# Kernel optimization log

Measured on AMD Instinct MI355X. Metric: run time of the kernel, lower is better.

Reference implementation:

```python
import jax, jax.numpy as jnp
import numpy as np

NL, DM, DI, DS, DR, DC = 4, 1024, 2048, 16, 64, 4
B, L, DLOC, NC = 8, 224, 672, 10
EPS = 1e-5


def _rmsnorm(h, w):
    return h * jax.lax.rsqrt(jnp.mean(h * h, axis=-1, keepdims=True) + EPS) * w


def setup_inputs() -> dict:
    key = jax.random.key(0)
    ks = jax.random.split(key, 10)
    s = 0.02
    return dict(
        x=jax.random.normal(ks[0], (B, L, DLOC), jnp.float32),
        w_proj=jax.random.normal(ks[1], (DLOC, DM), jnp.float32) * s,
        b_proj=jnp.zeros((DM,), jnp.float32),
        norm_w=jnp.ones((NL, DM), jnp.float32),
        w_in=jax.random.normal(ks[2], (NL, DM, 2 * DI), jnp.float32) * s,
        w_conv=jax.random.normal(ks[3], (NL, DI, DC), jnp.float32) * s,
        b_conv=jnp.zeros((NL, DI), jnp.float32),
        w_x=jax.random.normal(ks[4], (NL, DI, DR + 2 * DS), jnp.float32) * s,
        w_dt=jax.random.normal(ks[5], (NL, DR, DI), jnp.float32) * s,
        b_dt=jax.random.normal(ks[6], (NL, DI), jnp.float32) * 0.1,
        A_log=jnp.broadcast_to(jnp.log(jnp.arange(1, DS + 1, dtype=jnp.float32)), (NL, DI, DS)) + jnp.zeros((NL, DI, DS), jnp.float32),
        Dp=jnp.ones((NL, DI), jnp.float32),
        w_out=jax.random.normal(ks[7], (NL, DI, DM), jnp.float32) * s,
        final_norm_w=jnp.ones((DM,), jnp.float32),
        w_fc=jax.random.normal(ks[8], (DM, NC), jnp.float32) * s,
        b_fc=jnp.zeros((NC,), jnp.float32),
    )


def reference(x, w_proj, b_proj, norm_w, w_in, w_conv, b_conv, w_x, w_dt, b_dt, A_log, Dp, w_out, final_norm_w, w_fc, b_fc):
    # input_proj: (B,L,DLOC) -> (B,L,DM)
    h = x @ w_proj + b_proj
    for l in range(NL):
        xn = _rmsnorm(h, norm_w[l])
        xz = xn @ w_in[l]                      # (B,L,2*DI)
        xp, z = jnp.split(xz, 2, axis=-1)
        # causal depthwise conv1d along L, kernel size DC
        xpad = jnp.pad(xp, ((0, 0), (DC - 1, 0), (0, 0)))
        xc = sum(xpad[:, k:k + L, :] * w_conv[l][:, k] for k in range(DC)) + b_conv[l]
        xc = jax.nn.silu(xc)
        x_dbl = xc @ w_x[l]                    # (B,L,DR+2*DS)
        dtr, Bm, Cm = jnp.split(x_dbl, [DR, DR + DS], axis=-1)
        dt = jax.nn.softplus(dtr @ w_dt[l] + b_dt[l])   # (B,L,DI)
        A = -jnp.exp(A_log[l])                 # (DI,DS)
        xs = (jnp.swapaxes(dt, 0, 1), jnp.swapaxes(Bm, 0, 1),
              jnp.swapaxes(Cm, 0, 1), jnp.swapaxes(xc, 0, 1))

        def step(hs, inp):
            dt_t, B_t, C_t, u_t = inp          # (B,DI),(B,DS),(B,DS),(B,DI)
            dA = jnp.exp(dt_t[:, :, None] * A)                        # (B,DI,DS)
            hs = dA * hs + (dt_t * u_t)[:, :, None] * B_t[:, None, :]
            y = jnp.einsum('bds,bs->bd', hs, C_t)
            return hs, y

        h0 = jnp.zeros((B, DI, DS), x.dtype)
        _, ys = jax.lax.scan(step, h0, xs)     # ys: (L,B,DI)
        y = jnp.swapaxes(ys, 0, 1) + Dp[l] * xc
        y = y * jax.nn.silu(z)
        h = h + y @ w_out[l]
    h = _rmsnorm(h, final_norm_w)
    pooled = h[:, -1, :]                       # last-token pooling
    return pooled @ w_fc + b_fc                # (B,NC)
```

## Files before the change

### kernel.cpp

```cpp
#include <hip/hip_runtime.h>
#include <hip/hip_bf16.h>
#include <hip/hip_fp16.h>
#include <math.h>

#define NL 4
#define DM 1024
#define DI 2048
#define DS 16
#define DR 64
#define DC 4
#define B_ 8
#define L_ 224
#define DLOC 672
#define NC 10
#define EPS 1e-5f

#define ROWS (B_ * L_)
#define NCHK 14
#define CHS 16

typedef unsigned short u16;
typedef __attribute__((ext_vector_type(8))) short bf16x8;
typedef __attribute__((ext_vector_type(4))) float f32x4;
typedef __attribute__((address_space(1))) const void gvoid_t;
typedef __attribute__((address_space(3))) void lvoid_t;

__device__ __forceinline__ u16 f2bf(float f) {
  union { float f; unsigned int u; } v;
  v.f = f;
  unsigned int u = v.u;
  return (u16)((u + 0x7fffu + ((u >> 16) & 1u)) >> 16);
}

__device__ __forceinline__ void load4h(const __half* p, float* o) {
  uint2 r = *(const uint2*)p;
  __half2 h0 = *(__half2*)&r.x;
  __half2 h1 = *(__half2*)&r.y;
  float2 f0 = __half22float2(h0);
  float2 f1 = __half22float2(h1);
  o[0] = f0.x; o[1] = f0.y; o[2] = f1.x; o[3] = f1.y;
}

template <int ACC, int BROW, int TSTORE, int ACT, int SPLITK, typename OT>
__global__ __launch_bounds__(256) void gemm_bt_mfma(
    const u16* __restrict__ A, const u16* __restrict__ Bt,
    const float* __restrict__ bias, OT* __restrict__ C, int K, int lda,
    int ldb, int ldc) {
  if (SPLITK) {
    A += (size_t)blockIdx.z * SPLITK;
    Bt += (size_t)blockIdx.z * SPLITK;
  }
  __shared__ __align__(16) u16 As[2][128 * 32];
  __shared__ __align__(16) u16 Bs[2][128 * 32];
  const int tid = threadIdx.x;
  const int lane = tid & 63;
  const int wv = tid >> 6;
  const int n0 = blockIdx.x * 128;
  const int m0 = blockIdx.y * 128;
  const int wm0 = (wv & 1) * 64;
  const int wn0 = (wv >> 1) * 64;
  const int quad = lane >> 4;
  const int l16 = lane & 15;

  const int srow = wv * 32 + (lane >> 2);
  const int scol = (lane & 3) * 8;
  const u16* ga0 = A + (size_t)(m0 + srow) * lda + scol;
  const u16* ga1 = ga0 + (size_t)16 * lda;
  const u16* gb0 = Bt + (size_t)(n0 + srow) * ldb + scol;
  const u16* gb1 = gb0 + (size_t)16 * ldb;
  const int lo0 = (wv * 32) * 32;
  const int lo1 = (wv * 32 + 16) * 32;

  f32x4 acc[4][4] = {};

  auto STAGE = [&](int buf, int kk) {
    __builtin_amdgcn_global_load_lds((gvoid_t*)(ga0 + kk),
                                     (lvoid_t*)&As[buf][lo0], 16, 0, 0);
    __builtin_amdgcn_global_load_lds((gvoid_t*)(ga1 + kk),
                                     (lvoid_t*)&As[buf][lo1], 16, 0, 0);
    __builtin_amdgcn_global_load_lds((gvoid_t*)(gb0 + kk),
                                     (lvoid_t*)&Bs[buf][lo0], 16, 0, 0);
    __builtin_amdgcn_global_load_lds((gvoid_t*)(gb1 + kk),
                                     (lvoid_t*)&Bs[buf][lo1], 16, 0, 0);
  };

  const int NT = K >> 5;
  STAGE(0, 0);
  __syncthreads();
  for (int t = 0; t < NT; ++t) {
    const int cur = t & 1;
    if (t + 1 < NT) STAGE(cur ^ 1, (t + 1) << 5);
    bf16x8 af[4], bfr[4];
#pragma unroll
    for (int i = 0; i < 4; i++)
      af[i] = *(const bf16x8*)&As[cur][(wm0 + i * 16 + l16) * 32 + quad * 8];
#pragma unroll
    for (int j = 0; j < 4; j++)
      bfr[j] = *(const bf16x8*)&Bs[cur][(wn0 + j * 16 + l16) * 32 + quad * 8];
#pragma unroll
    for (int i = 0; i < 4; i++)
#pragma unroll
      for (int j = 0; j < 4; j++)
        acc[i][j] = __builtin_amdgcn_mfma_f32_16x16x32_bf16(af[i], bfr[j],
                                                            acc[i][j], 0, 0, 0);
    __syncthreads();
  }

#pragma unroll
  for (int i = 0; i < 4; i++) {
#pragma unroll
    for (int j = 0; j < 4; j++) {
      const int col = n0 + wn0 + j * 16 + l16;
      const int rowb = m0 + wm0 + i * 16 + quad * 4;
      if (TSTORE) {
        __half* Ch = (__half*)C;
        union { __half2 h[2]; uint2 u; } pk;
        pk.h[0].x = __float2half(acc[i][j][0]);
        pk.h[0].y = __float2half(acc[i][j][1]);
        pk.h[1].x = __float2half(acc[i][j][2]);
        pk.h[1].y = __float2half(acc[i][j][3]);
        *(uint2*)(Ch + (size_t)col * ldc + rowb) = pk.u;
      } else {
        float bv = 0.f;
        if (BROW == 1) bv = bias[col];
#pragma unroll
        for (int r = 0; r < 4; r++) {
          float v = acc[i][j][r] + bv;
          if (BROW == 2) v += bias[rowb + r];
          if (ACT == 1) v = (v > 20.f) ? v : log1pf(expf(v));
          OT* p = C + (size_t)(rowb + r) * ldc + col;
          if (ACC == 2) {
            atomicAdd((float*)p, v);
          } else {
            if (ACC == 1) v += (float)*p;
            *p = (OT)v;
          }
        }
      }
    }
  }
}

__device__ __forceinline__ void transpose_cvt_body(
    const float* __restrict__ src, u16* __restrict__ dst, int K, int N,
    int bx, int by, int tid) {
  __shared__ float t[32][33];
  const int n0 = bx * 32;
  const int k0 = by * 32;
  const int c = tid & 31;
  const int r = tid >> 5;
#pragma unroll
  for (int rr = 0; rr < 4; rr++)
    t[r + rr * 8][c] = src[(size_t)(k0 + r + rr * 8) * N + n0 + c];
  __syncthreads();
#pragma unroll
  for (int rr = 0; rr < 4; rr++)
    dst[(size_t)(n0 + r + rr * 8) * K + k0 + c] = f2bf(t[c][r + rr * 8]);
}

__global__ __launch_bounds__(256) void transpose_cvt_kernel(
    const float* __restrict__ src, u16* __restrict__ dst, int K, int N) {
  transpose_cvt_body(src, dst, K, N, blockIdx.x, blockIdx.y, threadIdx.x);
}

__global__ __launch_bounds__(256) void prep_weights_kernel(
    const float* __restrict__ w_in_l, const float* __restrict__ w_out_l,
    const float* __restrict__ w_x_l, const float* __restrict__ w_dt_l,
    u16* __restrict__ winT, u16* __restrict__ woutT, u16* __restrict__ w_x16,
    u16* __restrict__ w_dt16) {
  int bid = blockIdx.x;
  if (bid < 4096) {
    transpose_cvt_body(w_in_l, winT, DM, 2 * DI, bid & 127, bid >> 7,
                       threadIdx.x);
  } else if (bid < 6144) {
    bid -= 4096;
    transpose_cvt_body(w_out_l, woutT, DI, DM, bid & 31, bid >> 5,
                       threadIdx.x);
  } else if (bid < 6336) {
    bid -= 6144;
    transpose_cvt_body(w_x_l, w_x16, DI, 96, bid % 3, bid / 3, threadIdx.x);
  } else {
    bid -= 6336;
    transpose_cvt_body(w_dt_l, w_dt16, DR, DI, bid & 63, bid >> 6,
                       threadIdx.x);
  }
}

__global__ __launch_bounds__(256) void cvt_kernel(const float* __restrict__ src,
                                                  u16* __restrict__ dst) {
  const int i = blockIdx.x * 256 + threadIdx.x;
  const float4 v = ((const float4*)src)[i];
  ushort4 o;
  o.x = f2bf(v.x);
  o.y = f2bf(v.y);
  o.z = f2bf(v.z);
  o.w = f2bf(v.w);
  ((ushort4*)dst)[i] = o;
}

__global__ __launch_bounds__(256) void init_bias_kernel(
    const float* __restrict__ b, float* __restrict__ h) {
  const int i = blockIdx.x * 256 + threadIdx.x;
  const float4 v = ((const float4*)b)[i & (DM / 4 - 1)];
  ((float4*)h)[i] = v;
}

__global__ __launch_bounds__(256) void rmsnorm_kernel(
    const float* __restrict__ h, const float* __restrict__ w,
    u16* __restrict__ out) {
  const int row = blockIdx.x;
  const int tid = threadIdx.x;
  const float4 v = *(const float4*)(h + (size_t)row * DM + tid * 4);
  float ss = v.x * v.x + v.y * v.y + v.z * v.z + v.w * v.w;
#pragma unroll
  for (int off = 32; off > 0; off >>= 1) ss += __shfl_xor(ss, off);
  __shared__ float red[4];
  if ((tid & 63) == 0) red[tid >> 6] = ss;
  __syncthreads();
  float tot = red[0] + red[1] + red[2] + red[3];
  const float inv = rsqrtf(tot / (float)DM + EPS);
  const float4 wv = *(const float4*)(w + tid * 4);
  ushort4 o;
  o.x = f2bf(v.x * inv * wv.x);
  o.y = f2bf(v.y * inv * wv.y);
  o.z = f2bf(v.z * inv * wv.z);
  o.w = f2bf(v.w * inv * wv.w);
  *(ushort4*)(out + (size_t)row * DM + tid * 4) = o;
}

__global__ __launch_bounds__(256) void conv_silu_tile_kernel(
    const __half* __restrict__ xpT, const float* __restrict__ wc,
    const float* __restrict__ bc, __half* __restrict__ uT,
    u16* __restrict__ u16rm) {
  __shared__ u16 tile[32][33];
  const int tid = threadIdx.x;
  const int d0 = blockIdx.x * 32;
  const int r0 = blockIdx.y * 32;
  const int dl = tid >> 3;
  const int rq = (tid & 7) * 4;
  const int d = d0 + dl;
  const int r = r0 + rq;
  const int t = r % L_;
  const __half* row = xpT + (size_t)d * ROWS + r;
  float v[4];
  load4h(row, v);
  float p0 = 0.f, p1 = 0.f, p2 = 0.f;
  if (t > 0) {
    p0 = __half2float(row[-3]);
    p1 = __half2float(row[-2]);
    p2 = __half2float(row[-1]);
  }
  const float w0 = wc[d * 4 + 0], w1 = wc[d * 4 + 1], w2 = wc[d * 4 + 2],
              w3 = wc[d * 4 + 3];
  const float bb = bc[d];
  float o[4];
  float s;
  s = bb + p0 * w0 + p1 * w1 + p2 * w2 + v[0] * w3; o[0] = s / (1.f + expf(-s));
  s = bb + p1 * w0 + p2 * w1 + v[0] * w2 + v[1] * w3; o[1] = s / (1.f + expf(-s));
  s = bb + p2 * w0 + v[0] * w1 + v[1] * w2 + v[2] * w3; o[2] = s / (1.f + expf(-s));
  s = bb + v[0] * w0 + v[1] * w1 + v[2] * w2 + v[3] * w3; o[3] = s / (1.f + expf(-s));
  union { __half2 h[2]; uint2 u; } pk;
  pk.h[0].x = __float2half(o[0]); pk.h[0].y = __float2half(o[1]);
  pk.h[1].x = __float2half(o[2]); pk.h[1].y = __float2half(o[3]);
  *(uint2*)(uT + (size_t)d * ROWS + r) = pk.u;
#pragma unroll
  for (int i = 0; i < 4; i++) tile[rq + i][dl] = f2bf(o[i]);
  __syncthreads();
  const int rl = tid >> 3;
  const int dq = (tid & 7) * 4;
  ushort4 ov;
  ov.x = tile[rl][dq + 0];
  ov.y = tile[rl][dq + 1];
  ov.z = tile[rl][dq + 2];
  ov.w = tile[rl][dq + 3];
  *(ushort4*)(u16rm + (size_t)(r0 + rl) * DI + d0 + dq) = ov;
}

__global__ __launch_bounds__(64) void scan_state_kernel(
    const __half* __restrict__ dtT, const __half* __restrict__ uT,
    const float* __restrict__ xdblT, const float* __restrict__ A_log,
    float* __restrict__ S, float* __restrict__ sumdt) {
  __shared__ float Bsh[CHS][20];
  const int lane = threadIdx.x;
  const int c = blockIdx.x, g = blockIdx.y, b = blockIdx.z;
  const int d = (g << 6) + lane;
  const size_t tbase = (size_t)d * ROWS + (size_t)b * L_ + c * CHS;
  union HU { uint4 v[2]; __half h[16]; };
  HU dtb, ub;
  dtb.v[0] = *(const uint4*)(dtT + tbase);
  dtb.v[1] = *(const uint4*)(dtT + tbase + 8);
  ub.v[0] = *(const uint4*)(uT + tbase);
  ub.v[1] = *(const uint4*)(uT + tbase + 8);
  {
    const int s = lane >> 2, t0 = (lane & 3) * 4;
    const float4 bv = *(const float4*)(xdblT + (size_t)(DR + s) * ROWS +
                                       (size_t)b * L_ + c * CHS + t0);
    Bsh[t0 + 0][s] = bv.x;
    Bsh[t0 + 1][s] = bv.y;
    Bsh[t0 + 2][s] = bv.z;
    Bsh[t0 + 3][s] = bv.w;
  }
  float A2[DS];
  const float* al = A_log + (size_t)d * DS;
#pragma unroll
  for (int s = 0; s < DS; s++) A2[s] = -expf(al[s]) * 1.44269504f;
  __syncthreads();

  float hs[DS];
#pragma unroll
  for (int s = 0; s < DS; s++) hs[s] = 0.f;
  float cd = 0.f;
#pragma unroll
  for (int t = 0; t < CHS; t++) {
    const float dtv = __half2float(dtb.h[t]);
    const float uu = __half2float(ub.h[t]);
    const float du = dtv * uu;
    cd += dtv;
    const float4 B0 = *(const float4*)&Bsh[t][0];
    const float4 B1 = *(const float4*)&Bsh[t][4];
    const float4 B2 = *(const float4*)&Bsh[t][8];
    const float4 B3 = *(const float4*)&Bsh[t][12];
    auto upd = [&](int s0, float4 Bq) {
      hs[s0 + 0] = fmaf(hs[s0 + 0], exp2f(dtv * A2[s0 + 0]), du * Bq.x);
      hs[s0 + 1] = fmaf(hs[s0 + 1], exp2f(dtv * A2[s0 + 1]), du * Bq.y);
      hs[s0 + 2] = fmaf(hs[s0 + 2], exp2f(dtv * A2[s0 + 2]), du * Bq.z);
      hs[s0 + 3] = fmaf(hs[s0 + 3], exp2f(dtv * A2[s0 + 3]), du * Bq.w);
    };
    upd(0, B0); upd(4, B1); upd(8, B2); upd(12, B3);
  }
  float* Sp = S + (((size_t)c * B_ + b) * DI + d) * DS;
#pragma unroll
  for (int s = 0; s < DS; s++) Sp[s] = hs[s];
  sumdt[((size_t)c * B_ + b) * DI + d] = cd;
}

__global__ __launch_bounds__(256) void scan_combine_kernel(
    float* __restrict__ S, const float* __restrict__ sumdt,
    const float* __restrict__ A_log) {
  const int idx = blockIdx.x * 256 + threadIdx.x;
  const int s = idx & 15;
  const int d = (idx >> 4) & (DI - 1);
  const int b = idx >> 15;
  const float A2 = -expf(A_log[(size_t)d * DS + s]) * 1.44269504f;
  float hv = 0.f;
#pragma unroll
  for (int c = 0; c < NCHK; c++) {
    const size_t base = ((size_t)c * B_ + b) * DI + d;
    const size_t ix = base * DS + s;
    const float Sc = S[ix];
    const float Dc = exp2f(A2 * sumdt[base]);
    S[ix] = hv;
    hv = fmaf(Dc, hv, Sc);
  }
}

__global__ __launch_bounds__(64) void scan_apply_kernel(
    const __half* __restrict__ dtT, const __half* __restrict__ uT,
    const __half* __restrict__ zT, const float* __restrict__ xdblT,
    const float* __restrict__ A_log, const float* __restrict__ Dp,
    const float* __restrict__ HS, u16* __restrict__ y16) {
  __shared__ float bcs[CHS][36];
  __shared__ u16 ytile[CHS][72];
  const int lane = threadIdx.x;
  const int c = blockIdx.x, g = blockIdx.y, b = blockIdx.z;
  const int d = (g << 6) + lane;
  const size_t tbase = (size_t)d * ROWS + (size_t)b * L_ + c * CHS;
  union HU { uint4 v[2]; __half h[16]; };
  HU dtb, ub, zb;
  dtb.v[0] = *(const uint4*)(dtT + tbase);
  dtb.v[1] = *(const uint4*)(dtT + tbase + 8);
  ub.v[0] = *(const uint4*)(uT + tbase);
  ub.v[1] = *(const uint4*)(uT + tbase + 8);
  zb.v[0] = *(const uint4*)(zT + tbase);
  zb.v[1] = *(const uint4*)(zT + tbase + 8);
  {
    const int s = lane >> 1, t0 = (lane & 1) * 8;
    const float* src =
        xdblT + (size_t)(DR + s) * ROWS + (size_t)b * L_ + c * CHS + t0;
    const float4 v0 = *(const float4*)src;
    const float4 v1 = *(const float4*)(src + 4);
    bcs[t0 + 0][s] = v0.x; bcs[t0 + 1][s] = v0.y;
    bcs[t0 + 2][s] = v0.z; bcs[t0 + 3][s] = v0.w;
    bcs[t0 + 4][s] = v1.x; bcs[t0 + 5][s] = v1.y;
    bcs[t0 + 6][s] = v1.z; bcs[t0 + 7][s] = v1.w;
  }
  float A2[DS];
  const float* al = A_log + (size_t)d * DS;
#pragma unroll
  for (int s = 0; s < DS; s++) A2[s] = -expf(al[s]) * 1.44269504f;
  float hs[DS];
  const float* hp = HS + (((size_t)c * B_ + b) * DI + d) * DS;
#pragma unroll
  for (int s = 0; s < DS; s++) hs[s] = hp[s];
  const float Dpd = Dp[d];
  __syncthreads();

#pragma unroll
  for (int t = 0; t < CHS; t++) {
    const float dtv = __half2float(dtb.h[t]);
    const float uu = __half2float(ub.h[t]);
    const float zz = __half2float(zb.h[t]);
    const float du = dtv * uu;
    const float4 B0 = *(const float4*)&bcs[t][0];
    const float4 B1 = *(const float4*)&bcs[t][4];
    const float4 B2 = *(const float4*)&bcs[t][8];
    const float4 B3 = *(const float4*)&bcs[t][12];
    const float4 C0 = *(const float4*)&bcs[t][16];
    const float4 C1 = *(const float4*)&bcs[t][20];
    const float4 C2 = *(const float4*)&bcs[t][24];
    const float4 C3 = *(const float4*)&bcs[t][28];
    float p0 = 0.f, p1 = 0.f, p2 = 0.f, p3 = 0.f;
    auto upd = [&](int s0, float4 Bq, float4 Cq) {
      hs[s0 + 0] = fmaf(hs[s0 + 0], exp2f(dtv * A2[s0 + 0]), du * Bq.x);
      p0 = fmaf(hs[s0 + 0], Cq.x, p0);
      hs[s0 + 1] = fmaf(hs[s0 + 1], exp2f(dtv * A2[s0 + 1]), du * Bq.y);
      p1 = fmaf(hs[s0 + 1], Cq.y, p1);
      hs[s0 + 2] = fmaf(hs[s0 + 2], exp2f(dtv * A2[s0 + 2]), du * Bq.z);
      p2 = fmaf(hs[s0 + 2], Cq.z, p2);
      hs[s0 + 3] = fmaf(hs[s0 + 3], exp2f(dtv * A2[s0 + 3]), du * Bq.w);
      p3 = fmaf(hs[s0 + 3], Cq.w, p3);
    };
    upd(0, B0, C0); upd(4, B1, C1); upd(8, B2, C2); upd(12, B3, C3);
    float y = fmaf(Dpd, uu, (p0 + p1) + (p2 + p3));
    const float e = exp2f(-zz * 1.44269504f);
    y *= zz * __builtin_amdgcn_rcpf(1.f + e);
    ytile[t][lane] = f2bf(y);
  }
  __syncthreads();
  const int row = lane >> 2;
  const int seg = (lane & 3) * 16;
  u16* dst =
      y16 + ((size_t)b * L_ + c * CHS + row) * DI + (g << 6) + seg;
  *(uint4*)dst = *(const uint4*)&ytile[row][seg];
  *(uint4*)(dst + 8) = *(const uint4*)&ytile[row][seg + 8];
}

__global__ __launch_bounds__(256) void final_kernel(
    const float* __restrict__ h, const float* __restrict__ fnw,
    const float* __restrict__ w_fc, const float* __restrict__ b_fc,
    float* __restrict__ out) {
  const int b = blockIdx.x;
  const int tid = threadIdx.x;
  const size_t row = ((size_t)b * L_ + (L_ - 1)) * DM;
  const float4 v = *(const float4*)(h + row + tid * 4);
  float ss = v.x * v.x + v.y * v.y + v.z * v.z + v.w * v.w;
#pragma unroll
  for (int off = 32; off > 0; off >>= 1) ss += __shfl_xor(ss, off);
  __shared__ float red[4];
  if ((tid & 63) == 0) red[tid >> 6] = ss;
  __syncthreads();
  float tot = red[0] + red[1] + red[2] + red[3];
  const float inv = rsqrtf(tot / (float)DM + EPS);
  const float4 wv = *(const float4*)(fnw + tid * 4);
  float hn[4] = {v.x * inv * wv.x, v.y * inv * wv.y, v.z * inv * wv.z,
                 v.w * inv * wv.w};
  float partial[NC];
#pragma unroll
  for (int j = 0; j < NC; j++) partial[j] = 0.f;
#pragma unroll
  for (int e = 0; e < 4; e++) {
    const int dd = tid * 4 + e;
#pragma unroll
    for (int j = 0; j < NC; j++)
      partial[j] = fmaf(hn[e], w_fc[dd * NC + j], partial[j]);
  }
  __shared__ float red2[256][NC];
  for (int j = 0; j < NC; j++) red2[tid][j] = partial[j];
  __syncthreads();
  for (int stride = 128; stride > 0; stride >>= 1) {
    if (tid < stride)
      for (int j = 0; j < NC; j++) red2[tid][j] += red2[tid + stride][j];
    __syncthreads();
  }
  if (tid < NC) out[b * NC + tid] = red2[0][tid] + b_fc[tid];
}

extern "C" void kernel_launch(void* const* d_in, const int* in_sizes, int n_in,
                              void* d_out, int out_size, void* d_ws,
                              size_t ws_size, hipStream_t stream) {
  const float* x = (const float*)d_in[0];
  const float* w_proj = (const float*)d_in[1];
  const float* b_proj = (const float*)d_in[2];
  const float* norm_w = (const float*)d_in[3];
  const float* w_in = (const float*)d_in[4];
  const float* w_conv = (const float*)d_in[5];
  const float* b_conv = (const float*)d_in[6];
  const float* w_x = (const float*)d_in[7];
  const float* w_dt = (const float*)d_in[8];
  const float* b_dt = (const float*)d_in[9];
  const float* A_log = (const float*)d_in[10];
  const float* Dp = (const float*)d_in[11];
  const float* w_out = (const float*)d_in[12];
  const float* fnw = (const float*)d_in[13];
  const float* w_fc = (const float*)d_in[14];
  const float* b_fc = (const float*)d_in[15];
  float* out = (float*)d_out;

  float* ws = (float*)d_ws;
  float* h = ws;
  float* p = h + 1835008;
  __half* xzT = (__half*)p;    p += 3670016;
  __half* uT = (__half*)p;     p += 1835008;
  __half* dtT = (__half*)p;    p += 1835008;
  float* xdblT = p;            p += 229376;
  u16* y16 = (u16*)p;          p += 1835008;
  u16* xn16 = y16;
  u16* u16rm = (u16*)p;        p += 1835008;
  float* Sbuf = p;             p += 3670016;
  float* sumdt = p;            p += 229376;
  u16* x16 = (u16*)p;          p += 602112;
  u16* wprojT = (u16*)p;       p += 344064;
  u16* winT = (u16*)p;         p += 2097152;
  u16* woutT = (u16*)p;        p += 1048576;
  u16* w_x16 = (u16*)p;        p += 131072;
  u16* w_dt16 = (u16*)p;       p += 65536;
  u16* dtr16 = (u16*)p;        p += 57344;

  const dim3 blk(256);

  cvt_kernel<<<ROWS * DLOC / 1024, blk, 0, stream>>>(x, x16);
  transpose_cvt_kernel<<<dim3(DM / 32, DLOC / 32), blk, 0, stream>>>(
      w_proj, wprojT, DLOC, DM);
  init_bias_kernel<<<ROWS * DM / 1024, blk, 0, stream>>>(b_proj, h);

  gemm_bt_mfma<2, 0, 0, 0, 224, float>
      <<<dim3(DM / 128, ROWS / 128, 3), blk, 0, stream>>>(
          x16, wprojT, nullptr, h, 224, DLOC, DLOC, DM);

  for (int l = 0; l < NL; l++) {
    const float* Al = A_log + (size_t)l * DI * DS;
    prep_weights_kernel<<<6464, blk, 0, stream>>>(
        w_in + (size_t)l * DM * 2 * DI, w_out + (size_t)l * DI * DM,
        w_x + (size_t)l * DI * 96, w_dt + (size_t)l * DR * DI, winT, woutT,
        w_x16, w_dt16);

    rmsnorm_kernel<<<ROWS, blk, 0, stream>>>(h, norm_w + (size_t)l * DM, xn16);
    gemm_bt_mfma<0, 0, 1, 0, 0, __half>
        <<<dim3(2 * DI / 128, ROWS / 128), blk, 0, stream>>>(
            xn16, winT, nullptr, (__half*)xzT, DM, DM, DM, ROWS);
    conv_silu_tile_kernel<<<dim3(DI / 32, ROWS / 32), blk, 0, stream>>>(
        xzT, w_conv + (size_t)l * DI * DC, b_conv + (size_t)l * DI, uT, u16rm);
    hipMemsetAsync(xdblT, 0, (size_t)128 * ROWS * sizeof(float), stream);
    gemm_bt_mfma<2, 0, 0, 0, 512, float>
        <<<dim3(ROWS / 128, 1, 4), blk, 0, stream>>>(
            w_x16, u16rm, nullptr, xdblT, 512, DI, DI, ROWS);
    transpose_cvt_kernel<<<dim3(ROWS / 32, DR / 32), blk, 0, stream>>>(
        xdblT, dtr16, DR, ROWS);
    gemm_bt_mfma<0, 2, 0, 1, 0, __half>
        <<<dim3(ROWS / 128, DI / 128), blk, 0, stream>>>(
            w_dt16, dtr16, b_dt + (size_t)l * DI, dtT, DR, DR, DR, ROWS);
    scan_state_kernel<<<dim3(NCHK, DI / 64, B_), dim3(64), 0, stream>>>(
        dtT, uT, xdblT, Al, Sbuf, sumdt);
    scan_combine_kernel<<<B_ * DI * DS / 256, blk, 0, stream>>>(Sbuf, sumdt,
                                                                Al);
    scan_apply_kernel<<<dim3(NCHK, DI / 64, B_), dim3(64), 0, stream>>>(
        dtT, uT, xzT + (size_t)DI * ROWS, xdblT, Al, Dp + (size_t)l * DI,
        Sbuf, y16);
    gemm_bt_mfma<2, 0, 0, 0, 512, float>
        <<<dim3(DM / 128, ROWS / 128, 4), blk, 0, stream>>>(
            y16, woutT, nullptr, h, 512, DI, DI, DM);
  }

  final_kernel<<<B_, blk, 0, stream>>>(h, fnw, w_fc, b_fc, out);
}
```

Measured before the change: 929.1 us.

## Merge weight prep into one launch, use power ladder for geometric A, deepen split-K

All input conversion, bias init and per-layer weight transposes now run in a single kernel launched once up front, with per-layer weight buffers, which removes four per-layer prep launches and lets prep work spread across more blocks. In the scan kernels, when A_log makes A an integer multiple ladder (A[s] = (s+1)*A[0]), the 16 exp2 calls per step are replaced by one exp2 plus repeated multiplications, with a runtime check that falls back to the exp2 loop otherwise. The x_dbl GEMM split-K goes from 4 to 16 slices to expose more parallelism. The power ladder can drift slightly from exact exp, and the per-layer weight copies need more workspace.

```diff
diff --git a/kernel.cpp b/kernel.cpp
--- a/kernel.cpp
+++ b/kernel.cpp
@@ -39,6 +39,15 @@
   float2 f0 = __half22float2(h0);
   float2 f1 = __half22float2(h1);
   o[0] = f0.x; o[1] = f0.y; o[2] = f1.x; o[3] = f1.y;
+}
+
+__device__ __forceinline__ void pow_ladder(float a1, float* dA) {
+  const float a2 = a1 * a1, a4 = a2 * a2, a8 = a4 * a4;
+  dA[0] = a1;  dA[1] = a2;       dA[2] = a2 * a1;  dA[3] = a4;
+  dA[4] = a4 * a1; dA[5] = a4 * a2; dA[6] = a4 * dA[2]; dA[7] = a8;
+  dA[8] = a8 * a1; dA[9] = a8 * a2; dA[10] = a8 * dA[2]; dA[11] = a8 * a4;
+  dA[12] = a8 * dA[4]; dA[13] = a8 * dA[5]; dA[14] = a8 * dA[6];
+  dA[15] = a8 * a8;
 }
 
 template <int ACC, int BROW, int TSTORE, int ACT, int SPLITK, typename OT>
@@ -163,46 +172,59 @@
   transpose_cvt_body(src, dst, K, N, blockIdx.x, blockIdx.y, threadIdx.x);
 }
 
-__global__ __launch_bounds__(256) void prep_weights_kernel(
-    const float* __restrict__ w_in_l, const float* __restrict__ w_out_l,
-    const float* __restrict__ w_x_l, const float* __restrict__ w_dt_l,
-    u16* __restrict__ winT, u16* __restrict__ woutT, u16* __restrict__ w_x16,
+__global__ __launch_bounds__(256) void prep_all_kernel(
+    const float* __restrict__ x, const float* __restrict__ w_proj,
+    const float* __restrict__ b_proj, const float* __restrict__ w_in,
+    const float* __restrict__ w_out, const float* __restrict__ w_x,
+    const float* __restrict__ w_dt, u16* __restrict__ x16,
+    u16* __restrict__ wprojT, float* __restrict__ h, u16* __restrict__ winT,
+    u16* __restrict__ woutT, u16* __restrict__ w_x16,
     u16* __restrict__ w_dt16) {
   int bid = blockIdx.x;
+  const int tid = threadIdx.x;
+  if (bid < 1176) {
+    const int i = bid * 256 + tid;
+    const float4 v = ((const float4*)x)[i];
+    ushort4 o;
+    o.x = f2bf(v.x); o.y = f2bf(v.y); o.z = f2bf(v.z); o.w = f2bf(v.w);
+    ((ushort4*)x16)[i] = o;
+    return;
+  }
+  bid -= 1176;
+  if (bid < 672) {
+    transpose_cvt_body(w_proj, wprojT, DLOC, DM, bid & 31, bid >> 5, tid);
+    return;
+  }
+  bid -= 672;
+  if (bid < 1792) {
+    const int i = bid * 256 + tid;
+    const float4 v = ((const float4*)b_proj)[i & (DM / 4 - 1)];
+    ((float4*)h)[i] = v;
+    return;
+  }
+  bid -= 1792;
+  const int l = bid / 6464;
+  bid -= l * 6464;
+  const float* w_in_l = w_in + (size_t)l * DM * 2 * DI;
+  const float* w_out_l = w_out + (size_t)l * DI * DM;
+  const float* w_x_l = w_x + (size_t)l * DI * 96;
+  const float* w_dt_l = w_dt + (size_t)l * DR * DI;
+  u16* winT_l = winT + (size_t)l * 4194304;
+  u16* woutT_l = woutT + (size_t)l * 2097152;
+  u16* w_x16_l = w_x16 + (size_t)l * 262144;
+  u16* w_dt16_l = w_dt16 + (size_t)l * 131072;
   if (bid < 4096) {
-    transpose_cvt_body(w_in_l, winT, DM, 2 * DI, bid & 127, bid >> 7,
-                       threadIdx.x);
+    transpose_cvt_body(w_in_l, winT_l, DM, 2 * DI, bid & 127, bid >> 7, tid);
   } else if (bid < 6144) {
     bid -= 4096;
-    transpose_cvt_body(w_out_l, woutT, DI, DM, bid & 31, bid >> 5,
-                       threadIdx.x);
+    transpose_cvt_body(w_out_l, woutT_l, DI, DM, bid & 31, bid >> 5, tid);
   } else if (bid < 6336) {
     bid -= 6144;
-    transpose_cvt_body(w_x_l, w_x16, DI, 96, bid % 3, bid / 3, threadIdx.x);
+    transpose_cvt_body(w_x_l, w_x16_l, DI, 96, bid % 3, bid / 3, tid);
   } else {
     bid -= 6336;
-    transpose_cvt_body(w_dt_l, w_dt16, DR, DI, bid & 63, bid >> 6,
-                       threadIdx.x);
-  }
-}
-
-__global__ __launch_bounds__(256) void cvt_kernel(const float* __restrict__ src,
-                                                  u16* __restrict__ dst) {
-  const int i = blockIdx.x * 256 + threadIdx.x;
-  const float4 v = ((const float4*)src)[i];
-  ushort4 o;
-  o.x = f2bf(v.x);
-  o.y = f2bf(v.y);
-  o.z = f2bf(v.z);
-  o.w = f2bf(v.w);
-  ((ushort4*)dst)[i] = o;
-}
-
-__global__ __launch_bounds__(256) void init_bias_kernel(
-    const float* __restrict__ b, float* __restrict__ h) {
-  const int i = blockIdx.x * 256 + threadIdx.x;
-  const float4 v = ((const float4*)b)[i & (DM / 4 - 1)];
-  ((float4*)h)[i] = v;
+    transpose_cvt_body(w_dt_l, w_dt16_l, DR, DI, bid & 63, bid >> 6, tid);
+  }
 }
 
 __global__ __launch_bounds__(256) void rmsnorm_kernel(
@@ -304,6 +326,11 @@
   const float* al = A_log + (size_t)d * DS;
 #pragma unroll
   for (int s = 0; s < DS; s++) A2[s] = -expf(al[s]) * 1.44269504f;
+  bool geo = true;
+#pragma unroll
+  for (int s = 1; s < DS; s++)
+    geo = geo &&
+          (fabsf(A2[s] - (float)(s + 1) * A2[0]) <= 1e-6f * fabsf(A2[s]));
   __syncthreads();
 
   float hs[DS];
@@ -316,17 +343,20 @@
     const float uu = __half2float(ub.h[t]);
     const float du = dtv * uu;
     cd += dtv;
-    const float4 B0 = *(const float4*)&Bsh[t][0];
-    const float4 B1 = *(const float4*)&Bsh[t][4];
-    const float4 B2 = *(const float4*)&Bsh[t][8];
-    const float4 B3 = *(const float4*)&Bsh[t][12];
-    auto upd = [&](int s0, float4 Bq) {
-      hs[s0 + 0] = fmaf(hs[s0 + 0], exp2f(dtv * A2[s0 + 0]), du * Bq.x);
-      hs[s0 + 1] = fmaf(hs[s0 + 1], exp2f(dtv * A2[s0 + 1]), du * Bq.y);
-      hs[s0 + 2] = fmaf(hs[s0 + 2], exp2f(dtv * A2[s0 + 2]), du * Bq.z);
-      hs[s0 + 3] = fmaf(hs[s0 + 3], exp2f(dtv * A2[s0 + 3]), du * Bq.w);
-    };
-    upd(0, B0); upd(4, B1); upd(8, B2); upd(12, B3);
+    float Bv[DS];
+    *(float4*)&Bv[0] = *(const float4*)&Bsh[t][0];
+    *(float4*)&Bv[4] = *(const float4*)&Bsh[t][4];
+    *(float4*)&Bv[8] = *(const float4*)&Bsh[t][8];
+    *(float4*)&Bv[12] = *(const float4*)&Bsh[t][12];
+    float dA[DS];
+    if (geo) {
+      pow_ladder(exp2f(dtv * A2[0]), dA);
+    } else {
+#pragma unroll
+      for (int s = 0; s < DS; s++) dA[s] = exp2f(dtv * A2[s]);
+    }
+#pragma unroll
+    for (int s = 0; s < DS; s++) hs[s] = fmaf(hs[s], dA[s], du * Bv[s]);
   }
   float* Sp = S + (((size_t)c * B_ + b) * DI + d) * DS;
 #pragma unroll
@@ -388,6 +418,11 @@
   const float* al = A_log + (size_t)d * DS;
 #pragma unroll
   for (int s = 0; s < DS; s++) A2[s] = -expf(al[s]) * 1.44269504f;
+  bool geo = true;
+#pragma unroll
+  for (int s = 1; s < DS; s++)
+    geo = geo &&
+          (fabsf(A2[s] - (float)(s + 1) * A2[0]) <= 1e-6f * fabsf(A2[s]));
   float hs[DS];
   const float* hp = HS + (((size_t)c * B_ + b) * DI + d) * DS;
 #pragma unroll
@@ -401,26 +436,34 @@
     const float uu = __half2float(ub.h[t]);
     const float zz = __half2float(zb.h[t]);
     const float du = dtv * uu;
-    const float4 B0 = *(const float4*)&bcs[t][0];
-    const float4 B1 = *(const float4*)&bcs[t][4];
-    const float4 B2 = *(const float4*)&bcs[t][8];
-    const float4 B3 = *(const float4*)&bcs[t][12];
-    const float4 C0 = *(const float4*)&bcs[t][16];
-    const float4 C1 = *(const float4*)&bcs[t][20];
-    const float4 C2 = *(const float4*)&bcs[t][24];
-    const float4 C3 = *(const float4*)&bcs[t][28];
+    float Bv[DS], Cv[DS];
+    *(float4*)&Bv[0] = *(const float4*)&bcs[t][0];
+    *(float4*)&Bv[4] = *(const float4*)&bcs[t][4];
+    *(float4*)&Bv[8] = *(const float4*)&bcs[t][8];
+    *(float4*)&Bv[12] = *(const float4*)&bcs[t][12];
+    *(float4*)&Cv[0] = *(const float4*)&bcs[t][16];
+    *(float4*)&Cv[4] = *(const float4*)&bcs[t][20];
+    *(float4*)&Cv[8] = *(const float4*)&bcs[t][24];
+    *(float4*)&Cv[12] = *(const float4*)&bcs[t][28];
+    float dA[DS];
+    if (geo) {
+      pow_ladder(exp2f(dtv * A2[0]), dA);
+    } else {
+#pragma unroll
+      for (int s = 0; s < DS; s++) dA[s] = exp2f(dtv * A2[s]);
+    }
     float p0 = 0.f, p1 = 0.f, p2 = 0.f, p3 = 0.f;
-    auto upd = [&](int s0, float4 Bq, float4 Cq) {
-      hs[s0 + 0] = fmaf(hs[s0 + 0], exp2f(dtv * A2[s0 + 0]), du * Bq.x);
-      p0 = fmaf(hs[s0 + 0], Cq.x, p0);
-      hs[s0 + 1] = fmaf(hs[s0 + 1], exp2f(dtv * A2[s0 + 1]), du * Bq.y);
-      p1 = fmaf(hs[s0 + 1], Cq.y, p1);
-      hs[s0 + 2] = fmaf(hs[s0 + 2], exp2f(dtv * A2[s0 + 2]), du * Bq.z);
-      p2 = fmaf(hs[s0 + 2], Cq.z, p2);
-      hs[s0 + 3] = fmaf(hs[s0 + 3], exp2f(dtv * A2[s0 + 3]), du * Bq.w);
-      p3 = fmaf(hs[s0 + 3], Cq.w, p3);
-    };
-    upd(0, B0, C0); upd(4, B1, C1); upd(8, B2, C2); upd(12, B3, C3);
+#pragma unroll
+    for (int s = 0; s < DS; s += 4) {
+      hs[s + 0] = fmaf(hs[s + 0], dA[s + 0], du * Bv[s + 0]);
+      p0 = fmaf(hs[s + 0], Cv[s + 0], p0);
+      hs[s + 1] = fmaf(hs[s + 1], dA[s + 1], du * Bv[s + 1]);
+      p1 = fmaf(hs[s + 1], Cv[s + 1], p1);
+      hs[s + 2] = fmaf(hs[s + 2], dA[s + 2], du * Bv[s + 2]);
+      p2 = fmaf(hs[s + 2], Cv[s + 2], p2);
+      hs[s + 3] = fmaf(hs[s + 3], dA[s + 3], du * Bv[s + 3]);
+      p3 = fmaf(hs[s + 3], Cv[s + 3], p3);
+    }
     float y = fmaf(Dpd, uu, (p0 + p1) + (p2 + p3));
     const float e = exp2f(-zz * 1.44269504f);
     y *= zz * __builtin_amdgcn_rcpf(1.f + e);
@@ -510,18 +553,17 @@
   float* sumdt = p;            p += 229376;
   u16* x16 = (u16*)p;          p += 602112;
   u16* wprojT = (u16*)p;       p += 344064;
-  u16* winT = (u16*)p;         p += 2097152;
-  u16* woutT = (u16*)p;        p += 1048576;
-  u16* w_x16 = (u16*)p;        p += 131072;
-  u16* w_dt16 = (u16*)p;       p += 65536;
+  u16* winT = (u16*)p;         p += 8388608;
+  u16* woutT = (u16*)p;        p += 4194304;
+  u16* w_x16 = (u16*)p;        p += 524288;
+  u16* w_dt16 = (u16*)p;       p += 262144;
   u16* dtr16 = (u16*)p;        p += 57344;
 
   const dim3 blk(256);
 
-  cvt_kernel<<<ROWS * DLOC / 1024, blk, 0, stream>>>(x, x16);
-  transpose_cvt_kernel<<<dim3(DM / 32, DLOC / 32), blk, 0, stream>>>(
-      w_proj, wprojT, DLOC, DM);
-  init_bias_kernel<<<ROWS * DM / 1024, blk, 0, stream>>>(b_proj, h);
+  prep_all_kernel<<<1176 + 672 + 1792 + 4 * 6464, blk, 0, stream>>>(
+      x, w_proj, b_proj, w_in, w_out, w_x, w_dt, x16, wprojT, h, winT, woutT,
+      w_x16, w_dt16);
 
   gemm_bt_mfma<2, 0, 0, 0, 224, float>
       <<<dim3(DM / 128, ROWS / 128, 3), blk, 0, stream>>>(
@@ -529,26 +571,26 @@
 
   for (int l = 0; l < NL; l++) {
     const float* Al = A_log + (size_t)l * DI * DS;
-    prep_weights_kernel<<<6464, blk, 0, stream>>>(
-        w_in + (size_t)l * DM * 2 * DI, w_out + (size_t)l * DI * DM,
-        w_x + (size_t)l * DI * 96, w_dt + (size_t)l * DR * DI, winT, woutT,
-        w_x16, w_dt16);
+    const u16* winT_l = winT + (size_t)l * 4194304;
+    const u16* woutT_l = woutT + (size_t)l * 2097152;
+    const u16* w_x16_l = w_x16 + (size_t)l * 262144;
+    const u16* w_dt16_l = w_dt16 + (size_t)l * 131072;
 
     rmsnorm_kernel<<<ROWS, blk, 0, stream>>>(h, norm_w + (size_t)l * DM, xn16);
     gemm_bt_mfma<0, 0, 1, 0, 0, __half>
         <<<dim3(2 * DI / 128, ROWS / 128), blk, 0, stream>>>(
-            xn16, winT, nullptr, (__half*)xzT, DM, DM, DM, ROWS);
+            xn16, winT_l, nullptr, (__half*)xzT, DM, DM, DM, ROWS);
     conv_silu_tile_kernel<<<dim3(DI / 32, ROWS / 32), blk, 0, stream>>>(
         xzT, w_conv + (size_t)l * DI * DC, b_conv + (size_t)l * DI, uT, u16rm);
     hipMemsetAsync(xdblT, 0, (size_t)128 * ROWS * sizeof(float), stream);
-    gemm_bt_mfma<2, 0, 0, 0, 512, float>
-        <<<dim3(ROWS / 128, 1, 4), blk, 0, stream>>>(
-            w_x16, u16rm, nullptr, xdblT, 512, DI, DI, ROWS);
+    gemm_bt_mfma<2, 0, 0, 0, 128, float>
+        <<<dim3(ROWS / 128, 1, 16), blk, 0, stream>>>(
+            w_x16_l, u16rm, nullptr, xdblT, 128, DI, DI, ROWS);
     transpose_cvt_kernel<<<dim3(ROWS / 32, DR / 32), blk, 0, stream>>>(
         xdblT, dtr16, DR, ROWS);
     gemm_bt_mfma<0, 2, 0, 1, 0, __half>
         <<<dim3(ROWS / 128, DI / 128), blk, 0, stream>>>(
-            w_dt16, dtr16, b_dt + (size_t)l * DI, dtT, DR, DR, DR, ROWS);
+            w_dt16_l, dtr16, b_dt + (size_t)l * DI, dtT, DR, DR, DR, ROWS);
     scan_state_kernel<<<dim3(NCHK, DI / 64, B_), dim3(64), 0, stream>>>(
         dtT, uT, xdblT, Al, Sbuf, sumdt);
     scan_combine_kernel<<<B_ * DI * DS / 256, blk, 0, stream>>>(Sbuf, sumdt,
@@ -558,7 +600,7 @@
         Sbuf, y16);
     gemm_bt_mfma<2, 0, 0, 0, 512, float>
         <<<dim3(DM / 128, ROWS / 128, 4), blk, 0, stream>>>(
-            y16, woutT, nullptr, h, 512, DI, DI, DM);
+            y16, woutT_l, nullptr, h, 512, DI, DI, DM);
   }
 
   final_kernel<<<B_, blk, 0, stream>>>(h, fnw, w_fc, b_fc, out);
```

Result: slower. 1.350 ms (+45.3%).
